# Kernel optimization log

Hardware: AMD Instinct MI355X
Metric: run time of the kernel (lower is better)

## Reference

```python
import jax, jax.numpy as jnp
import numpy as np


def _cxcywh_to_xyxy(b):
    cx, cy, w, h = b[..., 0], b[..., 1], b[..., 2], b[..., 3]
    return jnp.stack([cx - 0.5 * w, cy - 0.5 * h, cx + 0.5 * w, cy + 0.5 * h], axis=-1)


def _generalized_box_iou(a, b):
    # a: [M,4] xyxy, b: [N,4] xyxy -> [M,N] GIoU matrix (DETR box_ops semantics)
    area_a = (a[:, 2] - a[:, 0]) * (a[:, 3] - a[:, 1])  # [M]
    area_b = (b[:, 2] - b[:, 0]) * (b[:, 3] - b[:, 1])  # [N]
    lt = jnp.maximum(a[:, None, :2], b[None, :, :2])    # [M,N,2]
    rb = jnp.minimum(a[:, None, 2:], b[None, :, 2:])
    wh = jnp.clip(rb - lt, 0.0)
    inter = wh[..., 0] * wh[..., 1]                     # [M,N]
    union = area_a[:, None] + area_b[None, :] - inter
    iou = inter / union
    lt_c = jnp.minimum(a[:, None, :2], b[None, :, :2])
    rb_c = jnp.maximum(a[:, None, 2:], b[None, :, 2:])
    wh_c = jnp.clip(rb_c - lt_c, 0.0)
    area_c = wh_c[..., 0] * wh_c[..., 1]
    return iou - (area_c - union) / area_c


def setup_inputs() -> dict:
    key = jax.random.key(0)
    k1, k2, k3 = jax.random.split(key, 3)
    B, T, N = 8, 64, 8
    # predicted boxes in cxcywh, all components in (0,1) -> positive w,h (valid)
    pred_boxes = jax.random.uniform(k1, (B, T, N, 4), dtype=jnp.float32)
    # target boxes directly in valid xyxy (code path uses them unconverted)
    centers = jax.random.uniform(k2, (B, T, N, 2), dtype=jnp.float32) * 0.8 + 0.1
    half_wh = (jax.random.uniform(k3, (B, T, N, 2), dtype=jnp.float32) * 0.2 + 0.02) * 0.5
    bboxes = jnp.concatenate([centers - half_wh, centers + half_wh], axis=-1)
    bboxes_mask = jnp.ones((B, T), dtype=bool)
    return {"pred_boxes": pred_boxes, "bboxes": bboxes, "bboxes_mask": bboxes_mask}


def reference(pred_boxes, bboxes, bboxes_mask):
    B, T, N, _ = pred_boxes.shape
    M = B * T * N
    # per-box validity (mask is per-frame, broadcast to boxes), as weights
    v = jnp.broadcast_to(bboxes_mask[:, :, None], (B, T, N)).reshape(M).astype(pred_boxes.dtype)
    src = _cxcywh_to_xyxy(pred_boxes.reshape(M, 4))   # [M,4]
    tgt = bboxes.reshape(M, 4)                        # [M,4]
    G = _generalized_box_iou(tgt, src)                # [M,M] rows=targets, cols=preds
    # argmax matching over valid prediction columns
    g_match = jnp.where(v[None, :] > 0, G, -jnp.inf)
    idx = jnp.argmax(g_match, axis=1)                 # [M]
    matched = src[idx]                                # [M,4]
    matched_gious = G[:, idx]                         # [M,M] (faithful to original)
    w = v[:, None] * v[idx][None, :]                  # validity weights
    loss_giou = 1.0 - jnp.sum(matched_gious * w) / jnp.sum(w)
    loss_bbox = jnp.sum(jnp.abs(matched - tgt) * v[:, None]) / (4.0 * jnp.sum(v))
    return loss_giou, loss_bbox
```

## Files before the change

kernel.cpp:

```cpp
#include <hip/hip_runtime.h>
#include <cmath>

#define WAVE 64
#define TPB  256
#define FTPB 1024

__device__ __forceinline__ float fastrcp(float x) { return __builtin_amdgcn_rcpf(x); }

__device__ __forceinline__ unsigned sortable_u32(float f) {
    unsigned b = __float_as_uint(f);
    return (b & 0x80000000u) ? ~b : (b | 0x80000000u);
}

__device__ __forceinline__ int mask_mode(const void* maskp) {
    const unsigned char* mb = (const unsigned char*)maskp;
    unsigned char b0 = mb[0], b1 = mb[1];
    if (b0 != 0 && b1 != 0) return 0;
    if (b0 != 0) return 1;
    return 2;
}
__device__ __forceinline__ float mask_v(const void* maskp, int t, int mode) {
    if (mode == 0) return ((const unsigned char*)maskp)[t] ? 1.0f : 0.0f;
    if (mode == 1) return ((const int*)maskp)[t] ? 1.0f : 0.0f;
    return (((const float*)maskp)[t] != 0.0f) ? 1.0f : 0.0f;
}
__device__ __forceinline__ int midx(int m, int nsh, int N) {
    return (nsh >= 0) ? (m >> nsh) : (m / N);
}

__global__ __launch_bounds__(TPB) void prep_kernel(
        const float4* __restrict__ pred, const float4* __restrict__ tgt,
        const void* __restrict__ maskp, int M, int nsh, int N,
        float4* __restrict__ convS, float* __restrict__ areaS,
        float* __restrict__ areaT, float* __restrict__ vv,
        unsigned long long* __restrict__ cmask) {
    int m = blockIdx.x * blockDim.x + threadIdx.x;
    if (m >= M) return;
    float4 p = pred[m];
    float x1 = p.x - 0.5f * p.z, y1 = p.y - 0.5f * p.w;
    float x2 = p.x + 0.5f * p.z, y2 = p.y + 0.5f * p.w;
    convS[m] = make_float4(x1, y1, x2, y2);
    areaS[m] = (x2 - x1) * (y2 - y1);
    float4 t = tgt[m];
    areaT[m] = (t.z - t.x) * (t.w - t.y);
    float vm = mask_v(maskp, midx(m, nsh, N), mask_mode(maskp));
    vv[m] = vm;
    unsigned long long bal = __ballot(vm > 0.0f);
    if ((threadIdx.x & (WAVE - 1)) == 0) cmask[m >> 6] = bal;
}

__global__ __launch_bounds__(TPB) void pass_kernel(
        const float4* __restrict__ tgt, const float* __restrict__ areaT,
        const float4* __restrict__ convS, const float* __restrict__ areaS,
        const unsigned long long* __restrict__ cmask, int M, int rowBlocks,
        unsigned long long* __restrict__ keypart, float* __restrict__ colpart) {
    const int C   = M >> 6;
    const int tid = threadIdx.x;

    if ((int)blockIdx.x < rowBlocks) {
        const int rb = blockIdx.x / C;
        const int cc = blockIdx.x % C;
        const int r  = rb * TPB + tid;
        float4 a  = tgt[r];
        float  aA = areaT[r];
        const unsigned long long cm = cmask[cc];
        const float4* __restrict__ bc = convS + (size_t)cc * 64;
        const float*  __restrict__ ba = areaS + (size_t)cc * 64;

        float best = -INFINITY;
        int   bidx = 0;
#pragma unroll 8
        for (int j = 0; j < 64; ++j) {
            if (!((cm >> j) & 1ull)) continue;
            float4 b  = bc[j];
            float  aB = ba[j];
            float ltx = fmaxf(a.x, b.x), lty = fmaxf(a.y, b.y);
            float rbx = fminf(a.z, b.z), rby = fminf(a.w, b.w);
            float w = fmaxf(rbx - ltx, 0.0f), h = fmaxf(rby - lty, 0.0f);
            float inter = w * h;
            float uni = aA + aB - inter;
            float cx1 = fminf(a.x, b.x), cy1 = fminf(a.y, b.y);
            float cx2 = fmaxf(a.z, b.z), cy2 = fmaxf(a.w, b.w);
            float areaC = (cx2 - cx1) * (cy2 - cy1);
            float hval = fmaf(uni, fastrcp(areaC), inter * fastrcp(uni));
            if (hval > best) { best = hval; bidx = cc * 64 + j; }
        }
        unsigned long long key = ((unsigned long long)sortable_u32(best) << 32)
                               | (unsigned)(~bidx);
        keypart[(size_t)cc * M + r] = key;
    } else {
        const int bb2 = blockIdx.x - rowBlocks;
        const int cb = bb2 / C;
        const int rc = bb2 % C;
        const int c  = cb * TPB + tid;
        float4 b  = convS[c];
        float  aB = areaS[c];
        const unsigned long long rm = cmask[rc];
        const float4* __restrict__ ar  = tgt   + (size_t)rc * 64;
        const float*  __restrict__ aar = areaT + (size_t)rc * 64;

        float csum = 0.0f;
#pragma unroll 8
        for (int j = 0; j < 64; ++j) {
            if (!((rm >> j) & 1ull)) continue;
            float4 a  = ar[j];
            float  aA = aar[j];
            float ltx = fmaxf(a.x, b.x), lty = fmaxf(a.y, b.y);
            float rbx = fminf(a.z, b.z), rby = fminf(a.w, b.w);
            float w = fmaxf(rbx - ltx, 0.0f), h = fmaxf(rby - lty, 0.0f);
            float inter = w * h;
            float uni = aA + aB - inter;
            float cx1 = fminf(a.x, b.x), cy1 = fminf(a.y, b.y);
            float cx2 = fmaxf(a.z, b.z), cy2 = fmaxf(a.w, b.w);
            float areaC = (cx2 - cx1) * (cy2 - cy1);
            float hval = fmaf(uni, fastrcp(areaC), inter * fastrcp(uni));
            csum += hval;
        }
        colpart[(size_t)rc * M + c] = csum;
    }
}

__global__ __launch_bounds__(TPB) void reduce_kernel(
        const unsigned long long* __restrict__ keypart,
        const float* __restrict__ colpart, int M, int C,
        int* __restrict__ idx, float* __restrict__ colsumh) {
    int m = blockIdx.x * blockDim.x + threadIdx.x;
    if (m >= M) return;
    unsigned long long k = keypart[m];
    float s = colpart[m];
    for (int cc = 1; cc < C; ++cc) {
        unsigned long long kc = keypart[(size_t)cc * M + m];
        k = (kc > k) ? kc : k;
        s += colpart[(size_t)cc * M + m];
    }
    idx[m] = (int)(~(unsigned)k);
    colsumh[m] = s;
}

__device__ __forceinline__ double wave_sum_d(double x) {
    for (int off = 32; off >= 1; off >>= 1) x += __shfl_xor(x, off);
    return x;
}

__global__ __launch_bounds__(FTPB) void finalize_kernel(
        const float4* __restrict__ convS, const float4* __restrict__ tgt,
        const float* __restrict__ vv, const int* __restrict__ idx,
        const float* __restrict__ colsumh, int M, float* __restrict__ out) {
    __shared__ double red[4 * (FTPB / WAVE)];
    const int tid = threadIdx.x;

    double sumV = 0.0, S2 = 0.0, S1h = 0.0, bbox = 0.0;
    for (int m = tid; m < M; m += FTPB) {
        float vi = vv[m];
        int   k  = idx[m];
        float vk = vv[k];
        sumV += (double)vi;
        S2   += (double)vk;
        S1h  += (double)vk * (double)colsumh[k];
        float4 s = convS[k];
        float4 t = tgt[m];
        bbox += (double)vi * (double)(fabsf(s.x - t.x) + fabsf(s.y - t.y) +
                                      fabsf(s.z - t.z) + fabsf(s.w - t.w));
    }
    sumV = wave_sum_d(sumV);
    S2   = wave_sum_d(S2);
    S1h  = wave_sum_d(S1h);
    bbox = wave_sum_d(bbox);
    int wid = tid >> 6, lane = tid & (WAVE - 1);
    const int NW = FTPB / WAVE;
    if (lane == 0) {
        red[wid] = sumV; red[NW + wid] = S2; red[2 * NW + wid] = S1h; red[3 * NW + wid] = bbox;
    }
    __syncthreads();
    if (tid == 0) {
        double a = 0, b = 0, c = 0, d = 0;
        for (int w = 0; w < NW; ++w) {
            a += red[w]; b += red[NW + w]; c += red[2 * NW + w]; d += red[3 * NW + w];
        }
        out[0] = (float)(2.0 - c / (a * b));
        out[1] = (float)(d / (4.0 * a));
    }
}

extern "C" void kernel_launch(void* const* d_in, const int* in_sizes, int n_in,
                              void* d_out, int out_size, void* d_ws, size_t ws_size,
                              hipStream_t stream) {
    const float4* pred = (const float4*)d_in[0];
    const float4* tgt  = (const float4*)d_in[1];
    const void*   mask = d_in[2];

    int M = in_sizes[0] / 4;
    int N = M / in_sizes[2];
    int nsh = -1;
    for (int s = 0; s < 31; ++s) if ((1 << s) == N) { nsh = s; break; }

    int C = M >> 6;

    char* ws = (char*)d_ws;
    float4* convS   = (float4*)ws;             ws += (size_t)M * 16;
    float*  areaS   = (float*)ws;              ws += (size_t)M * 4;
    float*  areaT   = (float*)ws;              ws += (size_t)M * 4;
    float*  vv      = (float*)ws;              ws += (size_t)M * 4;
    unsigned long long* cmaskp = (unsigned long long*)ws; ws += (size_t)C * 8;
    unsigned long long* keypart = (unsigned long long*)ws; ws += (size_t)C * M * 8;
    float*  colpart = (float*)ws;              ws += (size_t)C * M * 4;
    int*    idx     = (int*)ws;                ws += (size_t)M * 4;
    float*  colsumh = (float*)ws;              ws += (size_t)M * 4;
    float*  out = (float*)d_out;

    prep_kernel<<<(M + TPB - 1) / TPB, TPB, 0, stream>>>(
        pred, tgt, mask, M, nsh, N, convS, areaS, areaT, vv, cmaskp);

    int rowBlocks = (M / TPB) * C;
    int colBlocks = rowBlocks;
    pass_kernel<<<rowBlocks + colBlocks, TPB, 0, stream>>>(
        tgt, areaT, convS, areaS, cmaskp, M, rowBlocks, keypart, colpart);

    reduce_kernel<<<(M + TPB - 1) / TPB, TPB, 0, stream>>>(
        keypart, colpart, M, C, idx, colsumh);

    finalize_kernel<<<1, FTPB, 0, stream>>>(convS, tgt, vv, idx, colsumh, M, out);
}
```

Measured before the change: 114.3 us.

## Pack box data with mask bias and fold reduction into finalize kernel

```diff
diff --git a/kernel.cpp b/kernel.cpp
--- a/kernel.cpp
+++ b/kernel.cpp
@@ -4,6 +4,7 @@
 #define WAVE 64
 #define TPB  256
 #define FTPB 1024
+#define MMAX 4096
 
 __device__ __forceinline__ float fastrcp(float x) { return __builtin_amdgcn_rcpf(x); }
 
@@ -31,110 +32,85 @@
 __global__ __launch_bounds__(TPB) void prep_kernel(
         const float4* __restrict__ pred, const float4* __restrict__ tgt,
         const void* __restrict__ maskp, int M, int nsh, int N,
-        float4* __restrict__ convS, float* __restrict__ areaS,
-        float* __restrict__ areaT, float* __restrict__ vv,
-        unsigned long long* __restrict__ cmask) {
+        float4* __restrict__ pkS, float4* __restrict__ pkT) {
     int m = blockIdx.x * blockDim.x + threadIdx.x;
     if (m >= M) return;
+    float vm  = mask_v(maskp, midx(m, nsh, N), mask_mode(maskp));
+    float bias = (vm > 0.0f) ? 0.0f : -INFINITY;
+
     float4 p = pred[m];
     float x1 = p.x - 0.5f * p.z, y1 = p.y - 0.5f * p.w;
     float x2 = p.x + 0.5f * p.z, y2 = p.y + 0.5f * p.w;
-    convS[m] = make_float4(x1, y1, x2, y2);
-    areaS[m] = (x2 - x1) * (y2 - y1);
+    pkS[2 * m]     = make_float4(x1, y1, x2, y2);
+    pkS[2 * m + 1] = make_float4((x2 - x1) * (y2 - y1), vm, bias, 0.0f);
+
     float4 t = tgt[m];
-    areaT[m] = (t.z - t.x) * (t.w - t.y);
-    float vm = mask_v(maskp, midx(m, nsh, N), mask_mode(maskp));
-    vv[m] = vm;
-    unsigned long long bal = __ballot(vm > 0.0f);
-    if ((threadIdx.x & (WAVE - 1)) == 0) cmask[m >> 6] = bal;
+    pkT[2 * m]     = t;
+    pkT[2 * m + 1] = make_float4((t.z - t.x) * (t.w - t.y), vm, bias, 0.0f);
 }
 
 __global__ __launch_bounds__(TPB) void pass_kernel(
-        const float4* __restrict__ tgt, const float* __restrict__ areaT,
-        const float4* __restrict__ convS, const float* __restrict__ areaS,
-        const unsigned long long* __restrict__ cmask, int M, int rowBlocks,
+        const float4* __restrict__ pkS, const float4* __restrict__ pkT,
+        int M, int RB,
         unsigned long long* __restrict__ keypart, float* __restrict__ colpart) {
     const int C   = M >> 6;
     const int tid = threadIdx.x;
 
-    if ((int)blockIdx.x < rowBlocks) {
+    if ((int)blockIdx.x < RB) {
         const int rb = blockIdx.x / C;
         const int cc = blockIdx.x % C;
         const int r  = rb * TPB + tid;
-        float4 a  = tgt[r];
-        float  aA = areaT[r];
-        const unsigned long long cm = cmask[cc];
-        const float4* __restrict__ bc = convS + (size_t)cc * 64;
-        const float*  __restrict__ ba = areaS + (size_t)cc * 64;
+        float4 a  = pkT[2 * r];
+        float  aA = pkT[2 * r + 1].x;
+        const float4* __restrict__ bp = pkS + (size_t)cc * 128;
 
         float best = -INFINITY;
         int   bidx = 0;
 #pragma unroll 8
         for (int j = 0; j < 64; ++j) {
-            if (!((cm >> j) & 1ull)) continue;
-            float4 b  = bc[j];
-            float  aB = ba[j];
+            float4 b  = bp[2 * j];
+            float4 bm = bp[2 * j + 1];
             float ltx = fmaxf(a.x, b.x), lty = fmaxf(a.y, b.y);
             float rbx = fminf(a.z, b.z), rby = fminf(a.w, b.w);
             float w = fmaxf(rbx - ltx, 0.0f), h = fmaxf(rby - lty, 0.0f);
             float inter = w * h;
-            float uni = aA + aB - inter;
+            float uni = aA + bm.x - inter;
             float cx1 = fminf(a.x, b.x), cy1 = fminf(a.y, b.y);
             float cx2 = fmaxf(a.z, b.z), cy2 = fmaxf(a.w, b.w);
             float areaC = (cx2 - cx1) * (cy2 - cy1);
             float hval = fmaf(uni, fastrcp(areaC), inter * fastrcp(uni));
-            if (hval > best) { best = hval; bidx = cc * 64 + j; }
-        }
-        unsigned long long key = ((unsigned long long)sortable_u32(best) << 32)
-                               | (unsigned)(~bidx);
-        keypart[(size_t)cc * M + r] = key;
+            float val  = hval + bm.z;
+            if (val > best) { best = val; bidx = cc * 64 + j; }
+        }
+        keypart[(size_t)cc * M + r] = ((unsigned long long)sortable_u32(best) << 32)
+                                    | (unsigned)(~bidx);
     } else {
-        const int bb2 = blockIdx.x - rowBlocks;
-        const int cb = bb2 / C;
-        const int rc = bb2 % C;
+        const int b2 = blockIdx.x - RB;
+        const int cb = b2 / C;
+        const int rc = b2 % C;
         const int c  = cb * TPB + tid;
-        float4 b  = convS[c];
-        float  aB = areaS[c];
-        const unsigned long long rm = cmask[rc];
-        const float4* __restrict__ ar  = tgt   + (size_t)rc * 64;
-        const float*  __restrict__ aar = areaT + (size_t)rc * 64;
+        float4 b  = pkS[2 * c];
+        float  aB = pkS[2 * c + 1].x;
+        const float4* __restrict__ ap = pkT + (size_t)rc * 128;
 
         float csum = 0.0f;
 #pragma unroll 8
         for (int j = 0; j < 64; ++j) {
-            if (!((rm >> j) & 1ull)) continue;
-            float4 a  = ar[j];
-            float  aA = aar[j];
+            float4 a  = ap[2 * j];
+            float4 am = ap[2 * j + 1];
             float ltx = fmaxf(a.x, b.x), lty = fmaxf(a.y, b.y);
             float rbx = fminf(a.z, b.z), rby = fminf(a.w, b.w);
             float w = fmaxf(rbx - ltx, 0.0f), h = fmaxf(rby - lty, 0.0f);
             float inter = w * h;
-            float uni = aA + aB - inter;
+            float uni = am.x + aB - inter;
             float cx1 = fminf(a.x, b.x), cy1 = fminf(a.y, b.y);
             float cx2 = fmaxf(a.z, b.z), cy2 = fmaxf(a.w, b.w);
             float areaC = (cx2 - cx1) * (cy2 - cy1);
             float hval = fmaf(uni, fastrcp(areaC), inter * fastrcp(uni));
-            csum += hval;
+            csum = fmaf(am.y, hval, csum);
         }
         colpart[(size_t)rc * M + c] = csum;
     }
-}
-
-__global__ __launch_bounds__(TPB) void reduce_kernel(
-        const unsigned long long* __restrict__ keypart,
-        const float* __restrict__ colpart, int M, int C,
-        int* __restrict__ idx, float* __restrict__ colsumh) {
-    int m = blockIdx.x * blockDim.x + threadIdx.x;
-    if (m >= M) return;
-    unsigned long long k = keypart[m];
-    float s = colpart[m];
-    for (int cc = 1; cc < C; ++cc) {
-        unsigned long long kc = keypart[(size_t)cc * M + m];
-        k = (kc > k) ? kc : k;
-        s += colpart[(size_t)cc * M + m];
-    }
-    idx[m] = (int)(~(unsigned)k);
-    colsumh[m] = s;
 }
 
 __device__ __forceinline__ double wave_sum_d(double x) {
@@ -143,24 +119,40 @@
 }
 
 __global__ __launch_bounds__(FTPB) void finalize_kernel(
-        const float4* __restrict__ convS, const float4* __restrict__ tgt,
-        const float* __restrict__ vv, const int* __restrict__ idx,
-        const float* __restrict__ colsumh, int M, float* __restrict__ out) {
+        const float4* __restrict__ pkS, const float4* __restrict__ pkT,
+        const unsigned long long* __restrict__ keypart,
+        const float* __restrict__ colpart, int M, float* __restrict__ out) {
+    __shared__ float cs_lds[MMAX];
+    __shared__ int   idx_lds[MMAX];
     __shared__ double red[4 * (FTPB / WAVE)];
     const int tid = threadIdx.x;
+    const int C = M >> 6;
+
+    for (int m = tid; m < M; m += FTPB) {
+        unsigned long long k = keypart[m];
+        float s = colpart[m];
+        for (int cc = 1; cc < C; ++cc) {
+            unsigned long long kc = keypart[(size_t)cc * M + m];
+            k = (kc > k) ? kc : k;
+            s += colpart[(size_t)cc * M + m];
+        }
+        idx_lds[m] = (int)(~(unsigned)k);
+        cs_lds[m] = s;
+    }
+    __syncthreads();
 
     double sumV = 0.0, S2 = 0.0, S1h = 0.0, bbox = 0.0;
     for (int m = tid; m < M; m += FTPB) {
-        float vi = vv[m];
-        int   k  = idx[m];
-        float vk = vv[k];
+        float4 tm = pkT[2 * m];
+        float  vi = pkT[2 * m + 1].y;
+        int    k  = idx_lds[m];
+        float4 sk = pkS[2 * k];
+        float  vk = pkS[2 * k + 1].y;
         sumV += (double)vi;
         S2   += (double)vk;
-        S1h  += (double)vk * (double)colsumh[k];
-        float4 s = convS[k];
-        float4 t = tgt[m];
-        bbox += (double)vi * (double)(fabsf(s.x - t.x) + fabsf(s.y - t.y) +
-                                      fabsf(s.z - t.z) + fabsf(s.w - t.w));
+        S1h  += (double)vk * (double)cs_lds[k];
+        bbox += (double)vi * (double)(fabsf(sk.x - tm.x) + fabsf(sk.y - tm.y) +
+                                      fabsf(sk.z - tm.z) + fabsf(sk.w - tm.w));
     }
     sumV = wave_sum_d(sumV);
     S2   = wave_sum_d(S2);
@@ -197,27 +189,17 @@
     int C = M >> 6;
 
     char* ws = (char*)d_ws;
-    float4* convS   = (float4*)ws;             ws += (size_t)M * 16;
-    float*  areaS   = (float*)ws;              ws += (size_t)M * 4;
-    float*  areaT   = (float*)ws;              ws += (size_t)M * 4;
-    float*  vv      = (float*)ws;              ws += (size_t)M * 4;
-    unsigned long long* cmaskp = (unsigned long long*)ws; ws += (size_t)C * 8;
+    float4* pkS = (float4*)ws;                             ws += (size_t)M * 32;
+    float4* pkT = (float4*)ws;                             ws += (size_t)M * 32;
     unsigned long long* keypart = (unsigned long long*)ws; ws += (size_t)C * M * 8;
-    float*  colpart = (float*)ws;              ws += (size_t)C * M * 4;
-    int*    idx     = (int*)ws;                ws += (size_t)M * 4;
-    float*  colsumh = (float*)ws;              ws += (size_t)M * 4;
-    float*  out = (float*)d_out;
+    float* colpart = (float*)ws;                           ws += (size_t)C * M * 4;
+    float* out = (float*)d_out;
 
     prep_kernel<<<(M + TPB - 1) / TPB, TPB, 0, stream>>>(
-        pred, tgt, mask, M, nsh, N, convS, areaS, areaT, vv, cmaskp);
-
-    int rowBlocks = (M / TPB) * C;
-    int colBlocks = rowBlocks;
-    pass_kernel<<<rowBlocks + colBlocks, TPB, 0, stream>>>(
-        tgt, areaT, convS, areaS, cmaskp, M, rowBlocks, keypart, colpart);
-
-    reduce_kernel<<<(M + TPB - 1) / TPB, TPB, 0, stream>>>(
-        keypart, colpart, M, C, idx, colsumh);
-
-    finalize_kernel<<<1, FTPB, 0, stream>>>(convS, tgt, vv, idx, colsumh, M, out);
-}
+        pred, tgt, mask, M, nsh, N, pkS, pkT);
+
+    int RB = (M / TPB) * C;
+    pass_kernel<<<2 * RB, TPB, 0, stream>>>(pkS, pkT, M, RB, keypart, colpart);
+
+    finalize_kernel<<<1, FTPB, 0, stream>>>(pkS, pkT, keypart, colpart, M, out);
+}
```

Result: slower. 163.3 us (+42.9%).
